# Kernel tuning notes

Measured on AMD Instinct MI355X. Metric: run time of the kernel, lower is better.

The kernel has to match this reference:

```python
import jax, jax.numpy as jnp
import numpy as np

NF = 128   # n_feature
NA = 200000  # n_atoms
B = 256    # n_molecules (batch_mask rows)


def setup_inputs() -> dict:
    key = jax.random.key(0)
    ks = jax.random.split(key, 20)
    p = lambda k, shape: jax.random.normal(k, shape, jnp.float32) * 0.05
    s = jax.random.normal(ks[0], (1, NA, NF), jnp.float32)
    v = jax.random.normal(ks[1], (1, NA, 3, NF), jnp.float32)
    pos = jax.random.normal(ks[2], (1, NA, 3), jnp.float32)
    # one-hot batch mask: each atom assigned to one of B molecules
    idx = jax.random.randint(ks[3], (NA,), 0, B)
    batch = (idx[None, :] == jnp.arange(B)[:, None]).astype(jnp.float32)[..., None]  # (B, NA, 1)
    inp = dict(s=s, v=v, pos=pos, batch=batch)
    i = 4
    for l in range(2):  # n_output = 2 GatedEquivariant blocks
        inp[f"u{l}_w"] = p(ks[i], (NF, NF)); i += 1
        inp[f"v{l}_w"] = p(ks[i], (NF, NF)); i += 1
        inp[f"a{l}_w1"] = p(ks[i], (NF, 2 * NF)); i += 1
        inp[f"a{l}_b1"] = p(ks[i], (NF,)); i += 1
        inp[f"a{l}_w2"] = p(ks[i], (2 * NF, NF)); i += 1
        inp[f"a{l}_b2"] = p(ks[i], (2 * NF,)); i += 1
    inp["out_w"] = p(ks[i], (1, NF)); i += 1
    inp["out_b"] = p(ks[i], (1,))
    return inp


def _gated(s, v, uw, vw, aw1, ab1, aw2, ab2):
    # v: (1, na, 3, f); nn.Linear acts on last dim with weight (out, in)
    v1 = jnp.einsum('banf,gf->bang', v, uw)
    v2 = jnp.einsum('banf,gf->bang', v, vw)
    norm = jnp.linalg.norm(v2 + 1e-8, ord=2, axis=-2)  # (1, na, f)
    h = jnp.concatenate([s, norm], axis=-1)            # (1, na, 2f)
    h = jax.nn.silu(h @ aw1.T + ab1) @ aw2.T + ab2     # (1, na, 2f)
    sg, ss = jnp.split(h, 2, axis=-1)
    return sg, v1 * ss[:, :, None, :]


def reference(s, v, pos, batch,
              u0_w, v0_w, a0_w1, a0_b1, a0_w2, a0_b2,
              u1_w, v1_w, a1_w1, a1_b1, a1_w2, a1_b2,
              out_w, out_b):
    s, v = _gated(s, v, u0_w, v0_w, a0_w1, a0_b1, a0_w2, a0_b2)
    s, v = _gated(s, v, u1_w, v1_w, a1_w1, a1_b1, a1_w2, a1_b2)
    s = s @ out_w.T + out_b  # (1, na, 1)
    # faithful dense broadcast-mask pooling: (B, na, 1) * (B, na, 1) summed over atoms
    y = (jnp.broadcast_to(s, (batch.shape[0],) + s.shape[1:]) * batch).sum(axis=-2)
    return y  # (B, 1)
```

## Files before the change

### kernel.cpp

```cpp
#include <hip/hip_runtime.h>
#include <hip/hip_bf16.h>
#include <math.h>

typedef __attribute__((ext_vector_type(4))) float  f32x4;
typedef __attribute__((ext_vector_type(8))) __bf16 bf16x8;
typedef __attribute__((ext_vector_type(4))) unsigned int u32x4;

__device__ __forceinline__ f32x4 MF(bf16x8 a, bf16x8 b, f32x4 c) {
    return __builtin_amdgcn_mfma_f32_16x16x32_bf16(a, b, c, 0, 0, 0);
}

__device__ __forceinline__ f32x4 zero4() { f32x4 z = {0.f, 0.f, 0.f, 0.f}; return z; }

__device__ __forceinline__ unsigned int pkbf(float lo, float hi) {
    unsigned int r;
    asm("v_cvt_pk_bf16_f32 %0, %1, %2" : "=v"(r) : "v"(lo), "v"(hi));
    return r;
}
__device__ __forceinline__ unsigned long long pk4(f32x4 x) {
    return (unsigned long long)pkbf(x[0], x[1]) | ((unsigned long long)pkbf(x[2], x[3]) << 32);
}

__device__ __forceinline__ unsigned short f2bu(float x) {
    __bf16 h = (__bf16)x;
    return __builtin_bit_cast(unsigned short, h);
}

__device__ __forceinline__ bf16x8 bfrag_g(const float* W, int ldk, int row, int k0) {
    const float* p = W + (size_t)row * ldk + k0;
    bf16x8 r;
#pragma unroll
    for (int e = 0; e < 8; ++e) r[e] = (__bf16)p[e];
    return r;
}

#define SET_SZ   20480
#define VIN_OFF  0
#define H_OFF    12288
#define S1_OFF   40960
#define RED_OFF  45056
#define LDS_BYTES 45568

__device__ __forceinline__ bf16x8 afrag(const unsigned char* base, int rb, int row, int kb) {
    u32x4 q = *(const u32x4*)(base + row * rb + (kb ^ ((row & 7) << 4)));
    return __builtin_bit_cast(bf16x8, q);
}

__global__ __launch_bounds__(512, 2) void eqsc_main(
    const float* __restrict__ S, const float* __restrict__ V,
    const float* __restrict__ u0w, const float* __restrict__ v0w,
    const float* __restrict__ a0w1, const float* __restrict__ a0b1,
    const float* __restrict__ a0w2, const float* __restrict__ a0b2,
    const float* __restrict__ u1w, const float* __restrict__ v1w,
    const float* __restrict__ a1w1, const float* __restrict__ a1b1,
    const float* __restrict__ a1w2, const float* __restrict__ a1b2,
    const float* __restrict__ outw, const float* __restrict__ outbp,
    float* __restrict__ sOut, int NT)
{
    __shared__ __align__(16) unsigned char lds[LDS_BYTES];
    const int tid  = threadIdx.x;
    const int lane = tid & 63;
    const int wv   = tid >> 6;
    const int l15  = lane & 15;
    const int lg   = lane >> 4;
    const int grow = wv * 16 + l15;
    const int kbb  = lg << 4;
    const int fb0  = wv * 16 + (lg << 2);
    const int erow = l15;
    const int eswz = (erow & 7) << 4;

    f32x4 wfv = zero4();
    float cf = 0.f;
    for (int g = 0; g < 128; ++g) {
        float og = outw[g];
        f32x4 w4 = *(const f32x4*)(a1w2 + g * 128 + fb0);
#pragma unroll
        for (int e = 0; e < 4; ++e) wfv[e] += w4[e] * og;
        cf += a1b2[g] * og;
    }
    cf += outbp[0];

    bf16x8 uw0f[4], vw0f[4], w2g0[4], w2s0[4], vw1f[4];
    bf16x8 w1f0[8], w1f1[8];
#pragma unroll
    for (int kt = 0; kt < 4; ++kt) {
        int k0 = kt * 32 + lg * 8;
        uw0f[kt] = bfrag_g(u0w, 128, grow, k0);
        vw0f[kt] = bfrag_g(v0w, 128, grow, k0);
        w2g0[kt] = bfrag_g(a0w2, 128, grow, k0);
        w2s0[kt] = bfrag_g(a0w2, 128, 128 + grow, k0);
        vw1f[kt] = bfrag_g(v1w, 128, grow, k0);
    }
#pragma unroll
    for (int kt = 0; kt < 8; ++kt) {
        int k0 = kt * 32 + lg * 8;
        w1f0[kt] = bfrag_g(a0w1, 256, grow, k0);
        w1f1[kt] = bfrag_g(a1w1, 256, grow, k0);
    }
    const f32x4 b1_0v = *(const f32x4*)(a0b1 + fb0);
    const f32x4 b2g0v = *(const f32x4*)(a0b2 + fb0);
    const f32x4 b2s0v = *(const f32x4*)(a0b2 + 128 + fb0);
    const f32x4 b1_1v = *(const f32x4*)(a1b1 + fb0);

    const int stride = gridDim.x;
    const int t0 = blockIdx.x;

    if (t0 < NT) {
        f32x4 vld[3], sld;
#pragma unroll
        for (int j = 0; j < 3; ++j) {
            int c = tid + (j << 9);
            int d = c >> 9, rem = c & 511;
            int row = rem >> 5, c4 = rem & 31;
            vld[j] = *(const f32x4*)(V + (((size_t)((t0 << 4) + row) * 3 + d) << 7) + (c4 << 2));
        }
        { int row = tid >> 5, c4 = tid & 31;
          sld = *(const f32x4*)(S + (((size_t)((t0 << 4) + row)) << 7) + (c4 << 2)); }
#pragma unroll
        for (int j = 0; j < 3; ++j) {
            int c = tid + (j << 9);
            int d = c >> 9, rem = c & 511;
            int row = rem >> 5, c4 = rem & 31;
            *(unsigned long long*)(lds + VIN_OFF + (d << 12) + row * 256 +
                                   ((c4 << 3) ^ ((row & 7) << 4))) = pk4(vld[j]);
        }
        { int row = tid >> 5, c4 = tid & 31;
          *(unsigned long long*)(lds + H_OFF + row * 512 +
                                 ((c4 << 3) ^ ((row & 7) << 4))) = pk4(sld); }
    }
    __syncthreads();

    int i = 0;
    for (int ty = t0; ty < NT + stride; ty += stride, ++i) {
        const bool yv = (ty < NT);
        const bool xv = (i > 0);
        const int  tz = ty + stride;
        const bool zv = (tz < NT);
        unsigned char* Lsy = lds + (i & 1) * SET_SZ;
        unsigned char* Lsx = lds + ((i & 1) ^ 1) * SET_SZ;

        f32x4 vld[3], sld;
        if (zv) {
#pragma unroll
            for (int j = 0; j < 3; ++j) {
                int c = tid + (j << 9);
                int d = c >> 9, rem = c & 511;
                int row = rem >> 5, c4 = rem & 31;
                vld[j] = *(const f32x4*)(V + (((size_t)((tz << 4) + row) * 3 + d) << 7) + (c4 << 2));
            }
            { int row = tid >> 5, c4 = tid & 31;
              sld = *(const f32x4*)(S + (((size_t)((tz << 4) + row)) << 7) + (c4 << 2)); }
        }

        f32x4 v1a[3];
        if (yv) {
            f32x4 n2 = zero4();
#pragma unroll
            for (int d = 0; d < 3; ++d) {
                f32x4 a1 = zero4(), a2 = zero4();
#pragma unroll
                for (int kt = 0; kt < 4; ++kt) {
                    bf16x8 a = afrag(Lsy + VIN_OFF + (d << 12), 256, l15, (kt << 6) + kbb);
                    a1 = MF(uw0f[kt], a, a1);
                    a2 = MF(vw0f[kt], a, a2);
                }
                v1a[d] = a1;
#pragma unroll
                for (int e = 0; e < 4; ++e) { float x = a2[e] + 1e-8f; n2[e] += x * x; }
            }
            f32x4 nr;
#pragma unroll
            for (int e = 0; e < 4; ++e) nr[e] = sqrtf(n2[e]);
            *(unsigned long long*)(Lsy + H_OFF + erow * 512 +
                ((256 + (fb0 << 1)) ^ eswz)) = pk4(nr);
        }
        if (xv) {
            f32x4 n2 = zero4();
#pragma unroll
            for (int d = 0; d < 3; ++d) {
                f32x4 acc = zero4();
#pragma unroll
                for (int kt = 0; kt < 4; ++kt)
                    acc = MF(vw1f[kt], afrag(Lsx + VIN_OFF + (d << 12), 256, l15, (kt << 6) + kbb),
                             acc);
#pragma unroll
                for (int e = 0; e < 4; ++e) { float x = acc[e] + 1e-8f; n2[e] += x * x; }
            }
            f32x4 nr;
#pragma unroll
            for (int e = 0; e < 4; ++e) nr[e] = sqrtf(n2[e]);
            *(unsigned long long*)(Lsx + H_OFF + erow * 512 +
                ((256 + (fb0 << 1)) ^ eswz)) = pk4(nr);
        }
        __syncthreads();

        if (yv) {
            f32x4 m = zero4();
#pragma unroll
            for (int kt = 0; kt < 8; ++kt)
                m = MF(w1f0[kt], afrag(Lsy + H_OFF, 512, l15, (kt << 6) + kbb), m);
            f32x4 y;
#pragma unroll
            for (int e = 0; e < 4; ++e) {
                float x = m[e] + b1_0v[e];
                y[e] = x / (1.f + __expf(-x));
            }
            *(unsigned long long*)(lds + S1_OFF + erow * 256 +
                ((fb0 << 1) ^ eswz)) = pk4(y);
        }
        if (xv) {
            f32x4 m = zero4();
#pragma unroll
            for (int kt = 0; kt < 8; ++kt)
                m = MF(w1f1[kt], afrag(Lsx + H_OFF, 512, l15, (kt << 6) + kbb), m);
            float p = 0.f;
#pragma unroll
            for (int e = 0; e < 4; ++e) {
                float x = m[e] + b1_1v[e];
                p += (x / (1.f + __expf(-x))) * wfv[e];
            }
            p += __shfl_xor(p, 16);
            p += __shfl_xor(p, 32);
            if (lane < 16)
                *((float*)(lds + RED_OFF) + (wv << 4) + lane) = p;
        }
        if (zv) {
#pragma unroll
            for (int j = 0; j < 3; ++j) {
                int c = tid + (j << 9);
                int d = c >> 9, rem = c & 511;
                int row = rem >> 5, c4 = rem & 31;
                *(unsigned long long*)(Lsx + VIN_OFF + (d << 12) + row * 256 +
                                       ((c4 << 3) ^ ((row & 7) << 4))) = pk4(vld[j]);
            }
        }
        __syncthreads();

        if (yv) {
            f32x4 sg = zero4(), ssa = zero4();
#pragma unroll
            for (int kt = 0; kt < 4; ++kt) {
                bf16x8 a = afrag(lds + S1_OFF, 256, l15, (kt << 6) + kbb);
                sg  = MF(w2g0[kt], a, sg);
                ssa = MF(w2s0[kt], a, ssa);
            }
            f32x4 g, ssv;
#pragma unroll
            for (int e = 0; e < 4; ++e) {
                g[e]   = sg[e] + b2g0v[e];
                ssv[e] = ssa[e] + b2s0v[e];
            }
            *(unsigned long long*)(Lsy + H_OFF + erow * 512 + ((fb0 << 1) ^ eswz)) = pk4(g);
#pragma unroll
            for (int d = 0; d < 3; ++d) {
                f32x4 vp;
#pragma unroll
                for (int e = 0; e < 4; ++e) vp[e] = v1a[d][e] * ssv[e];
                *(unsigned long long*)(Lsy + VIN_OFF + (d << 12) + erow * 256 +
                    ((fb0 << 1) ^ eswz)) = pk4(vp);
            }
        }
        if (zv) {
            int row = tid >> 5, c4 = tid & 31;
            *(unsigned long long*)(Lsx + H_OFF + row * 512 +
                                   ((c4 << 3) ^ ((row & 7) << 4))) = pk4(sld);
        }
        if (xv && tid < 16) {
            float s = 0.f;
#pragma unroll
            for (int w = 0; w < 8; ++w) s += *((float*)(lds + RED_OFF) + (w << 4) + tid);
            sOut[((ty - stride) << 4) + tid] = s + cf;
        }
        __syncthreads();
    }
}

__global__ __launch_bounds__(256) void eqsc_pool(const float* __restrict__ batch,
                                                 const float* __restrict__ s,
                                                 float* __restrict__ out,
                                                 int NA, int B, int CH)
{
    int b  = blockIdx.x % B;
    int ch = blockIdx.x / B;
    int a0 = ch * CH;
    int a1 = min(a0 + CH, NA);
    const float* br = batch + (size_t)b * NA;
    float acc = 0.f;
    for (int a = a0 + (threadIdx.x << 2); a < a1; a += 256 * 4) {
        f32x4 bb = *(const f32x4*)(br + a);
        f32x4 sv = *(const f32x4*)(s + a);
        acc += bb[0] * sv[0] + bb[1] * sv[1] + bb[2] * sv[2] + bb[3] * sv[3];
    }
#pragma unroll
    for (int off = 32; off > 0; off >>= 1) acc += __shfl_down(acc, off);
    __shared__ float wsum[4];
    if ((threadIdx.x & 63) == 0) wsum[threadIdx.x >> 6] = acc;
    __syncthreads();
    if (threadIdx.x == 0) atomicAdd(&out[b], wsum[0] + wsum[1] + wsum[2] + wsum[3]);
}

extern "C" void kernel_launch(void* const* d_in, const int* in_sizes, int n_in,
                              void* d_out, int out_size, void* d_ws, size_t ws_size,
                              hipStream_t stream)
{
    const float* S     = (const float*)d_in[0];
    const float* V     = (const float*)d_in[1];
    const float* batch = (const float*)d_in[3];
    const float* u0w   = (const float*)d_in[4];
    const float* v0w   = (const float*)d_in[5];
    const float* a0w1  = (const float*)d_in[6];
    const float* a0b1  = (const float*)d_in[7];
    const float* a0w2  = (const float*)d_in[8];
    const float* a0b2  = (const float*)d_in[9];
    const float* u1w   = (const float*)d_in[10];
    const float* v1w   = (const float*)d_in[11];
    const float* a1w1  = (const float*)d_in[12];
    const float* a1b1  = (const float*)d_in[13];
    const float* a1w2  = (const float*)d_in[14];
    const float* a1b2  = (const float*)d_in[15];
    const float* outw  = (const float*)d_in[16];
    const float* outb  = (const float*)d_in[17];

    const int NA = in_sizes[0] / 128;
    const int NT = NA / 16;
    const int B  = in_sizes[3] / NA;
    float* sAtom = (float*)d_ws;

    hipMemsetAsync(d_out, 0, (size_t)out_size * sizeof(float), stream);

    eqsc_main<<<256, 512, 0, stream>>>(S, V, u0w, v0w, a0w1, a0b1, a0w2, a0b2,
                                       u1w, v1w, a1w1, a1b1, a1w2, a1b2,
                                       outw, outb, sAtom, NT);

    const int CH  = 16384;
    const int NCH = (NA + CH - 1) / CH;
    eqsc_pool<<<B * NCH, 256, 0, stream>>>(batch, sAtom, (float*)d_out, NA, B, CH);
}
```

Baseline: 244.3 us.

## Deepen software pipeline to four stages and remove one barrier per tile

Restructures the persistent tile loop into a four-stage skewed pipeline. Gate projection and u-matmul now run one iteration after the norm stage, layer-2 MLP two iterations later, and the reduction write three iterations later. The change drops the third __syncthreads per iteration and spreads MFMA work more evenly between barriers. In exchange it uses more LDS (about 74KB versus 45KB), which may limit occupancy at two blocks per CU, and it recomputes the u-projection from a retained raw V buffer.

```diff
diff --git a/kernel.cpp b/kernel.cpp
--- a/kernel.cpp
+++ b/kernel.cpp
@@ -21,11 +21,6 @@
     return (unsigned long long)pkbf(x[0], x[1]) | ((unsigned long long)pkbf(x[2], x[3]) << 32);
 }
 
-__device__ __forceinline__ unsigned short f2bu(float x) {
-    __bf16 h = (__bf16)x;
-    return __builtin_bit_cast(unsigned short, h);
-}
-
 __device__ __forceinline__ bf16x8 bfrag_g(const float* W, int ldk, int row, int k0) {
     const float* p = W + (size_t)row * ldk + k0;
     bf16x8 r;
@@ -34,12 +29,13 @@
     return r;
 }
 
-#define SET_SZ   20480
-#define VIN_OFF  0
-#define H_OFF    12288
-#define S1_OFF   40960
-#define RED_OFF  45056
-#define LDS_BYTES 45568
+#define RAW(b)   ((b) * 12288)
+#define VPR      24576
+#define HB(b)    (36864 + (b) * 8192)
+#define HP(b)    (53248 + (b) * 8192)
+#define S1_OFF   69632
+#define RED_OFF  73728
+#define LDS_BYTES 74240
 
 __device__ __forceinline__ bf16x8 afrag(const unsigned char* base, int rb, int row, int kb) {
     u32x4 q = *(const u32x4*)(base + row * rb + (kb ^ ((row & 7) << 4)));
@@ -104,8 +100,9 @@
 
     const int stride = gridDim.x;
     const int t0 = blockIdx.x;
-
-    if (t0 < NT) {
+    const int NI = (NT > t0) ? ((NT - t0 + stride - 1) / stride) : 0;
+
+    if (NI > 0) {
         f32x4 vld[3], sld;
 #pragma unroll
         for (int j = 0; j < 3; ++j) {
@@ -121,23 +118,25 @@
             int c = tid + (j << 9);
             int d = c >> 9, rem = c & 511;
             int row = rem >> 5, c4 = rem & 31;
-            *(unsigned long long*)(lds + VIN_OFF + (d << 12) + row * 256 +
+            *(unsigned long long*)(lds + RAW(0) + (d << 12) + row * 256 +
                                    ((c4 << 3) ^ ((row & 7) << 4))) = pk4(vld[j]);
         }
         { int row = tid >> 5, c4 = tid & 31;
-          *(unsigned long long*)(lds + H_OFF + row * 512 +
+          *(unsigned long long*)(lds + HB(0) + row * 512 +
                                  ((c4 << 3) ^ ((row & 7) << 4))) = pk4(sld); }
     }
     __syncthreads();
 
-    int i = 0;
-    for (int ty = t0; ty < NT + stride; ty += stride, ++i) {
-        const bool yv = (ty < NT);
-        const bool xv = (i > 0);
-        const int  tz = ty + stride;
-        const bool zv = (tz < NT);
-        unsigned char* Lsy = lds + (i & 1) * SET_SZ;
-        unsigned char* Lsx = lds + ((i & 1) ^ 1) * SET_SZ;
+    for (int i = 0; i < NI + 3; ++i) {
+        const bool yv  = (i < NI);
+        const bool xv  = (i >= 1) && (i - 1 < NI);
+        const bool wvd = (i >= 2) && (i - 2 < NI);
+        const bool fvd = (i >= 3) && (i - 3 < NI);
+        const int  ty  = t0 + i * stride;
+        const int  tz  = ty + stride;
+        const bool zv  = (i + 1 < NI);
+        const int  rY  = i & 1;
+        const int  rX  = (i + 1) & 1;
 
         f32x4 vld[3], sld;
         if (zv) {
@@ -151,46 +150,56 @@
             { int row = tid >> 5, c4 = tid & 31;
               sld = *(const f32x4*)(S + (((size_t)((tz << 4) + row)) << 7) + (c4 << 2)); }
         }
-
-        f32x4 v1a[3];
+        if (fvd && tid < 16) {
+            float s = 0.f;
+#pragma unroll
+            for (int w = 0; w < 8; ++w) s += *((float*)(lds + RED_OFF) + (w << 4) + tid);
+            sOut[((t0 + (i - 3) * stride) << 4) + tid] = s + cf;
+        }
         if (yv) {
             f32x4 n2 = zero4();
 #pragma unroll
             for (int d = 0; d < 3; ++d) {
-                f32x4 a1 = zero4(), a2 = zero4();
-#pragma unroll
-                for (int kt = 0; kt < 4; ++kt) {
-                    bf16x8 a = afrag(Lsy + VIN_OFF + (d << 12), 256, l15, (kt << 6) + kbb);
-                    a1 = MF(uw0f[kt], a, a1);
-                    a2 = MF(vw0f[kt], a, a2);
-                }
-                v1a[d] = a1;
+                f32x4 a2 = zero4();
+#pragma unroll
+                for (int kt = 0; kt < 4; ++kt)
+                    a2 = MF(vw0f[kt], afrag(lds + RAW(rY) + (d << 12), 256, l15, (kt << 6) + kbb), a2);
 #pragma unroll
                 for (int e = 0; e < 4; ++e) { float x = a2[e] + 1e-8f; n2[e] += x * x; }
             }
             f32x4 nr;
 #pragma unroll
             for (int e = 0; e < 4; ++e) nr[e] = sqrtf(n2[e]);
-            *(unsigned long long*)(Lsy + H_OFF + erow * 512 +
+            *(unsigned long long*)(lds + HB(rY) + erow * 512 +
                 ((256 + (fb0 << 1)) ^ eswz)) = pk4(nr);
         }
         if (xv) {
-            f32x4 n2 = zero4();
+            f32x4 sg = zero4(), ssa = zero4();
+#pragma unroll
+            for (int kt = 0; kt < 4; ++kt) {
+                bf16x8 a = afrag(lds + S1_OFF, 256, l15, (kt << 6) + kbb);
+                sg  = MF(w2g0[kt], a, sg);
+                ssa = MF(w2s0[kt], a, ssa);
+            }
+            f32x4 g, ssv;
+#pragma unroll
+            for (int e = 0; e < 4; ++e) {
+                g[e]   = sg[e] + b2g0v[e];
+                ssv[e] = ssa[e] + b2s0v[e];
+            }
+            *(unsigned long long*)(lds + HP(rX) + erow * 512 + ((fb0 << 1) ^ eswz)) = pk4(g);
 #pragma unroll
             for (int d = 0; d < 3; ++d) {
-                f32x4 acc = zero4();
+                f32x4 u = zero4();
 #pragma unroll
                 for (int kt = 0; kt < 4; ++kt)
-                    acc = MF(vw1f[kt], afrag(Lsx + VIN_OFF + (d << 12), 256, l15, (kt << 6) + kbb),
-                             acc);
-#pragma unroll
-                for (int e = 0; e < 4; ++e) { float x = acc[e] + 1e-8f; n2[e] += x * x; }
-            }
-            f32x4 nr;
-#pragma unroll
-            for (int e = 0; e < 4; ++e) nr[e] = sqrtf(n2[e]);
-            *(unsigned long long*)(Lsx + H_OFF + erow * 512 +
-                ((256 + (fb0 << 1)) ^ eswz)) = pk4(nr);
+                    u = MF(uw0f[kt], afrag(lds + RAW(rX) + (d << 12), 256, l15, (kt << 6) + kbb), u);
+                f32x4 vp;
+#pragma unroll
+                for (int e = 0; e < 4; ++e) vp[e] = u[e] * ssv[e];
+                *(unsigned long long*)(lds + VPR + (d << 12) + erow * 256 +
+                    ((fb0 << 1) ^ eswz)) = pk4(vp);
+            }
         }
         __syncthreads();
 
@@ -198,21 +207,37 @@
             f32x4 m = zero4();
 #pragma unroll
             for (int kt = 0; kt < 8; ++kt)
-                m = MF(w1f0[kt], afrag(Lsy + H_OFF, 512, l15, (kt << 6) + kbb), m);
+                m = MF(w1f0[kt], afrag(lds + HB(rY), 512, l15, (kt << 6) + kbb), m);
             f32x4 y;
 #pragma unroll
             for (int e = 0; e < 4; ++e) {
                 float x = m[e] + b1_0v[e];
                 y[e] = x / (1.f + __expf(-x));
             }
-            *(unsigned long long*)(lds + S1_OFF + erow * 256 +
-                ((fb0 << 1) ^ eswz)) = pk4(y);
+            *(unsigned long long*)(lds + S1_OFF + erow * 256 + ((fb0 << 1) ^ eswz)) = pk4(y);
         }
         if (xv) {
+            f32x4 n2 = zero4();
+#pragma unroll
+            for (int d = 0; d < 3; ++d) {
+                f32x4 acc = zero4();
+#pragma unroll
+                for (int kt = 0; kt < 4; ++kt)
+                    acc = MF(vw1f[kt], afrag(lds + VPR + (d << 12), 256, l15, (kt << 6) + kbb), acc);
+#pragma unroll
+                for (int e = 0; e < 4; ++e) { float x = acc[e] + 1e-8f; n2[e] += x * x; }
+            }
+            f32x4 nr;
+#pragma unroll
+            for (int e = 0; e < 4; ++e) nr[e] = sqrtf(n2[e]);
+            *(unsigned long long*)(lds + HP(rX) + erow * 512 +
+                ((256 + (fb0 << 1)) ^ eswz)) = pk4(nr);
+        }
+        if (wvd) {
             f32x4 m = zero4();
 #pragma unroll
             for (int kt = 0; kt < 8; ++kt)
-                m = MF(w1f1[kt], afrag(Lsx + H_OFF, 512, l15, (kt << 6) + kbb), m);
+                m = MF(w1f1[kt], afrag(lds + HP(rY), 512, l15, (kt << 6) + kbb), m);
             float p = 0.f;
 #pragma unroll
             for (int e = 0; e < 4; ++e) {
@@ -230,46 +255,12 @@
                 int c = tid + (j << 9);
                 int d = c >> 9, rem = c & 511;
                 int row = rem >> 5, c4 = rem & 31;
-                *(unsigned long long*)(Lsx + VIN_OFF + (d << 12) + row * 256 +
+                *(unsigned long long*)(lds + RAW(rX) + (d << 12) + row * 256 +
                                        ((c4 << 3) ^ ((row & 7) << 4))) = pk4(vld[j]);
             }
-        }
-        __syncthreads();
-
-        if (yv) {
-            f32x4 sg = zero4(), ssa = zero4();
-#pragma unroll
-            for (int kt = 0; kt < 4; ++kt) {
-                bf16x8 a = afrag(lds + S1_OFF, 256, l15, (kt << 6) + kbb);
-                sg  = MF(w2g0[kt], a, sg);
-                ssa = MF(w2s0[kt], a, ssa);
-            }
-            f32x4 g, ssv;
-#pragma unroll
-            for (int e = 0; e < 4; ++e) {
-                g[e]   = sg[e] + b2g0v[e];
-                ssv[e] = ssa[e] + b2s0v[e];
-            }
-            *(unsigned long long*)(Lsy + H_OFF + erow * 512 + ((fb0 << 1) ^ eswz)) = pk4(g);
-#pragma unroll
-            for (int d = 0; d < 3; ++d) {
-                f32x4 vp;
-#pragma unroll
-                for (int e = 0; e < 4; ++e) vp[e] = v1a[d][e] * ssv[e];
-                *(unsigned long long*)(Lsy + VIN_OFF + (d << 12) + erow * 256 +
-                    ((fb0 << 1) ^ eswz)) = pk4(vp);
-            }
-        }
-        if (zv) {
-            int row = tid >> 5, c4 = tid & 31;
-            *(unsigned long long*)(Lsx + H_OFF + row * 512 +
-                                   ((c4 << 3) ^ ((row & 7) << 4))) = pk4(sld);
-        }
-        if (xv && tid < 16) {
-            float s = 0.f;
-#pragma unroll
-            for (int w = 0; w < 8; ++w) s += *((float*)(lds + RED_OFF) + (w << 4) + tid);
-            sOut[((ty - stride) << 4) + tid] = s + cf;
+            { int row = tid >> 5, c4 = tid & 31;
+              *(unsigned long long*)(lds + HB(rX) + row * 512 +
+                                     ((c4 << 3) ^ ((row & 7) << 4))) = pk4(sld); }
         }
         __syncthreads();
     }
```

Measured after the change: 295.4 us. +20.9%, slower.
